# Optimization experiments

Measured on AMD Instinct MI355X. Metric: run time of the kernel, lower is better.

## Reference

```python
import jax, jax.numpy as jnp
import numpy as np

N_NODES = 50000
N_EDGES = 800000
F_IN = 128
HIDDEN = 128
N_CLASSES = 40


def setup_inputs() -> dict:
    key = jax.random.key(0)
    ks = jax.random.split(key, 8)
    x = jax.random.normal(ks[0], (N_NODES, F_IN), dtype=jnp.float32)
    edge_index = jax.random.randint(ks[1], (2, N_EDGES), 0, N_NODES, dtype=jnp.int32)
    s_in = 1.0 / np.sqrt(F_IN)
    s_h = 1.0 / np.sqrt(HIDDEN)
    W1_l = jax.random.normal(ks[2], (F_IN, HIDDEN), jnp.float32) * s_in
    W1_r = jax.random.normal(ks[3], (F_IN, HIDDEN), jnp.float32) * s_in
    b1 = jnp.zeros((HIDDEN,), jnp.float32)
    W2_l = jax.random.normal(ks[4], (HIDDEN, N_CLASSES), jnp.float32) * s_h
    W2_r = jax.random.normal(ks[5], (HIDDEN, N_CLASSES), jnp.float32) * s_h
    b2 = jnp.zeros((N_CLASSES,), jnp.float32)
    return {"x": x, "edge_index": edge_index, "W1_l": W1_l, "W1_r": W1_r,
            "b1": b1, "W2_l": W2_l, "W2_r": W2_r, "b2": b2}


def _sage_conv(x, src, dst, W_l, W_r, b):
    # mean-aggregate neighbor features at dst, then linear transform + root weight
    msg = x[src]                                                  # [E, d] gather
    agg = jax.ops.segment_sum(msg, dst, num_segments=N_NODES)     # [N, d] scatter-add
    deg = jax.ops.segment_sum(jnp.ones((src.shape[0],), x.dtype), dst,
                              num_segments=N_NODES)
    agg = agg / jnp.maximum(deg, 1.0)[:, None]                    # mean aggregation
    return agg @ W_l + x @ W_r + b


def reference(x, edge_index, W1_l, W1_r, b1, W2_l, W2_r, b2):
    src, dst = edge_index[0], edge_index[1]
    h = jax.nn.relu(_sage_conv(x, src, dst, W1_l, W1_r, b1))
    # F.dropout(p=0.5, training=self.training) -> identity in eval mode
    out = jax.nn.relu(_sage_conv(h, src, dst, W2_l, W2_r, b2))
    return jax.nn.log_softmax(out, axis=-1)
```

## Files before the change

kernel.cpp:

```cpp
#include <hip/hip_runtime.h>

#define N_NODES 50000
#define N_EDGES 800000
#define F_IN 128
#define HIDDEN 128
#define N_CLASSES 40

#define NBUCKET 196
#define BUCKET_CAP 8192
#define BINA_CHUNK 4096
#define BINA_NBLK 196
#define PREP_ITEMS (N_NODES * 32 + 128 * 256 + 80 * 128)
#define PREP_NBLK (PREP_ITEMS / 256)

#define OFF_RS     0
#define OFF_BCNT   50004
#define OFF_INVDEG 100004
#define OFF_SRCS   150004
#define OFF_AB     950004
#define OFF_PB     950004
#define OFF_Q      2950004
#define OFF_BINS   7350004
#define OFF_HB     7350004
#define OFF_WT1    10550004
#define OFF_WT2    10566388

typedef short bf16x8 __attribute__((ext_vector_type(8)));
typedef float f32x4 __attribute__((ext_vector_type(4)));
typedef unsigned short u16x8 __attribute__((ext_vector_type(8)));
typedef unsigned short u16x4 __attribute__((ext_vector_type(4)));

static __device__ __forceinline__ unsigned short f2bf(float f) {
  unsigned int u = __builtin_bit_cast(unsigned int, f);
  u = (u + 0x7fffu + ((u >> 16) & 1u)) >> 16;
  return (unsigned short)u;
}
static __device__ __forceinline__ float bf2f(unsigned short s) {
  unsigned int u = ((unsigned int)s) << 16;
  return __builtin_bit_cast(float, u);
}

__global__ __launch_bounds__(256) void k_binA_prep(
    const int* __restrict__ src, const int* __restrict__ dst,
    int* __restrict__ bcnt, int* __restrict__ bins,
    const float* __restrict__ x, const float* __restrict__ W1l,
    const float* __restrict__ W1r, const float* __restrict__ W2l,
    const float* __restrict__ W2r, unsigned short* __restrict__ Ab,
    unsigned short* __restrict__ Wt1, unsigned short* __restrict__ Wt2) {
  if (blockIdx.x >= BINA_NBLK) {
    int idx = (blockIdx.x - BINA_NBLK) * 256 + threadIdx.x;
    if (idx < N_NODES * 32) {
      int row = idx >> 5, c4 = (idx & 31) << 2;
      const float4 v = *(const float4*)(x + (size_t)row * F_IN + c4);
      ushort4 o;
      o.x = f2bf(v.x); o.y = f2bf(v.y); o.z = f2bf(v.z); o.w = f2bf(v.w);
      *(ushort4*)(Ab + (size_t)row * 256 + 128 + c4) = o;
      return;
    }
    idx -= N_NODES * 32;
    if (idx < 128 * 256) {
      int n = idx >> 8, k = idx & 255;
      float v = (k < 128) ? W1l[(size_t)k * 128 + n]
                          : W1r[(size_t)(k - 128) * 128 + n];
      Wt1[(size_t)n * 256 + k] = f2bf(v);
    } else if (idx < 128 * 256 + 80 * 128) {
      int j = idx - 128 * 256;
      int n = j >> 7, k = j & 127;
      float v = (n < 40) ? W2l[(size_t)k * 40 + n]
                         : W2r[(size_t)k * 40 + (n - 40)];
      Wt2[(size_t)n * 128 + k] = f2bf(v);
    }
    return;
  }
  __shared__ int cnt[NBUCKET];
  __shared__ int excl[NBUCKET];
  __shared__ int cursor[NBUCKET];
  __shared__ int bbase[NBUCKET];
  __shared__ int sc[256];
  __shared__ int stage[BINA_CHUNK];
  __shared__ unsigned char bkt[BINA_CHUNK];
  int t = threadIdx.x;
  int e0 = blockIdx.x * BINA_CHUNK;
  int ne = N_EDGES - e0;
  if (ne > BINA_CHUNK) ne = BINA_CHUNK;
  if (t < NBUCKET) cnt[t] = 0;
  __syncthreads();
  for (int i = t; i < ne; i += 256) atomicAdd(&cnt[dst[e0 + i] >> 8], 1);
  __syncthreads();
  int v = (t < NBUCKET) ? cnt[t] : 0;
  sc[t] = v;
  __syncthreads();
  for (int off = 1; off < 256; off <<= 1) {
    int add = (t >= off) ? sc[t - off] : 0;
    __syncthreads();
    sc[t] += add;
    __syncthreads();
  }
  if (t < NBUCKET) {
    int ex = sc[t] - v;
    excl[t] = ex;
    cursor[t] = ex;
    bbase[t] = atomicAdd(&bcnt[t], v);
  }
  __syncthreads();
  for (int i = t; i < ne; i += 256) {
    int d = dst[e0 + i];
    int s = src[e0 + i];
    int b = d >> 8;
    int pos = atomicAdd(&cursor[b], 1);
    stage[pos] = ((d & 255) << 16) | s;
    bkt[pos] = (unsigned char)b;
  }
  __syncthreads();
  for (int i = t; i < ne; i += 256) {
    int b = bkt[i];
    bins[(size_t)b * BUCKET_CAP + bbase[b] + (i - excl[b])] = stage[i];
  }
}

__global__ __launch_bounds__(256) void k_binB(
    const int* __restrict__ bcnt, const int* __restrict__ bins,
    int* __restrict__ rs, int* __restrict__ srcs,
    float* __restrict__ invdeg) {
  __shared__ int sc[256];
  __shared__ int hist[256];
  __shared__ int cursor[256];
  int b = blockIdx.x;
  int t = threadIdx.x;
  sc[t] = (t < NBUCKET && t < b) ? bcnt[t] : 0;
  __syncthreads();
  for (int off = 128; off; off >>= 1) {
    if (t < off) sc[t] += sc[t + off];
    __syncthreads();
  }
  int base = sc[0];
  int cnt = bcnt[b];
  const int* bb = bins + (size_t)b * BUCKET_CAP;
  hist[t] = 0;
  __syncthreads();
  for (int i = t; i < cnt; i += 256) atomicAdd(&hist[bb[i] >> 16], 1);
  __syncthreads();
  int c = hist[t];
  sc[t] = c;
  __syncthreads();
  for (int off = 1; off < 256; off <<= 1) {
    int add = (t >= off) ? sc[t - off] : 0;
    __syncthreads();
    sc[t] += add;
    __syncthreads();
  }
  int lexcl = sc[t] - c;
  int node = b * 256 + t;
  if (node < N_NODES) {
    rs[node] = base + lexcl;
    invdeg[node] = 1.0f / (float)(c > 1 ? c : 1);
  }
  if (b == 0 && t == 0) rs[N_NODES] = N_EDGES;
  cursor[t] = lexcl;
  __syncthreads();
  for (int i = t; i < cnt; i += 256) {
    int v = bb[i];
    int pos = atomicAdd(&cursor[v >> 16], 1);
    srcs[base + pos] = v & 0xFFFF;
  }
}

__global__ __launch_bounds__(256) void k_gather1(
    const int* __restrict__ rs, const int* __restrict__ srcs,
    const float* __restrict__ invdeg, unsigned short* __restrict__ Ab) {
  int node = blockIdx.x * 4 + (threadIdx.x >> 6);
  int lane = threadIdx.x & 63;
  int slot = lane >> 4, li = lane & 15;
  if (node >= N_NODES) return;
  int beg = rs[node], end = rs[node + 1];
  float acc[8];
#pragma unroll
  for (int j = 0; j < 8; j++) acc[j] = 0.f;
  for (int i = beg + slot; i < end; i += 4) {
    int s = srcs[i];
    u16x8 v = *(const u16x8*)(Ab + (size_t)s * 256 + 128 + li * 8);
#pragma unroll
    for (int j = 0; j < 8; j++) acc[j] += bf2f(v[j]);
  }
#pragma unroll
  for (int off = 16; off <= 32; off <<= 1)
#pragma unroll
    for (int j = 0; j < 8; j++) acc[j] += __shfl_xor(acc[j], off, 64);
  if (slot == 0) {
    float inv = invdeg[node];
    u16x8 o;
#pragma unroll
    for (int j = 0; j < 8; j++) o[j] = f2bf(acc[j] * inv);
    *(u16x8*)(Ab + (size_t)node * 256 + li * 8) = o;
  }
}

__global__ __launch_bounds__(256) void k_l1(
    const unsigned short* __restrict__ Ab, const unsigned short* __restrict__ Wt1,
    const float* __restrict__ b1, unsigned short* __restrict__ hb) {
  int w = threadIdx.x >> 6, lane = threadIdx.x & 63;
  int r = lane & 15, quad = lane >> 4;
  int row0 = blockIdx.x * 64 + w * 16;
  int arow = row0 + r;
  if (arow >= N_NODES) arow = N_NODES - 1;
  const unsigned short* Ap = Ab + (size_t)arow * 256 + quad * 8;
  const unsigned short* Bp = Wt1 + (size_t)r * 256 + quad * 8;
  f32x4 acc[8];
#pragma unroll
  for (int n = 0; n < 8; n++) acc[n] = (f32x4){0.f, 0.f, 0.f, 0.f};
#pragma unroll
  for (int k0 = 0; k0 < 256; k0 += 32) {
    bf16x8 af = *(const bf16x8*)(Ap + k0);
#pragma unroll
    for (int n = 0; n < 8; n++) {
      bf16x8 bv = *(const bf16x8*)(Bp + (size_t)n * 16 * 256 + k0);
      acc[n] = __builtin_amdgcn_mfma_f32_16x16x32_bf16(af, bv, acc[n], 0, 0, 0);
    }
  }
  int crow0 = row0 + quad * 4;
#pragma unroll
  for (int n = 0; n < 8; n++) {
    int col = n * 16 + r;
    float bias = b1[col];
#pragma unroll
    for (int reg = 0; reg < 4; reg++) {
      int row = crow0 + reg;
      if (row < N_NODES)
        hb[(size_t)row * HIDDEN + col] = f2bf(fmaxf(acc[n][reg] + bias, 0.f));
    }
  }
}

__global__ __launch_bounds__(256) void k_pq(
    const unsigned short* __restrict__ hb, const unsigned short* __restrict__ Wt2,
    const float* __restrict__ b2, unsigned short* __restrict__ pb,
    float* __restrict__ q) {
  int w = threadIdx.x >> 6, lane = threadIdx.x & 63;
  int r = lane & 15, quad = lane >> 4;
  int row0 = blockIdx.x * 64 + w * 16;
  int arow = row0 + r;
  if (arow >= N_NODES) arow = N_NODES - 1;
  const unsigned short* Ap = hb + (size_t)arow * HIDDEN + quad * 8;
  const unsigned short* Bp = Wt2 + (size_t)r * 128 + quad * 8;
  f32x4 acc[5];
#pragma unroll
  for (int n = 0; n < 5; n++) acc[n] = (f32x4){0.f, 0.f, 0.f, 0.f};
#pragma unroll
  for (int k0 = 0; k0 < 128; k0 += 32) {
    bf16x8 af = *(const bf16x8*)(Ap + k0);
#pragma unroll
    for (int n = 0; n < 5; n++) {
      bf16x8 bv = *(const bf16x8*)(Bp + (size_t)n * 16 * 128 + k0);
      acc[n] = __builtin_amdgcn_mfma_f32_16x16x32_bf16(af, bv, acc[n], 0, 0, 0);
    }
  }
  int crow0 = row0 + quad * 4;
#pragma unroll
  for (int n = 0; n < 5; n++) {
    int col = n * 16 + r;
#pragma unroll
    for (int reg = 0; reg < 4; reg++) {
      int row = crow0 + reg;
      if (row < N_NODES) {
        float v = acc[n][reg];
        if (col < N_CLASSES)
          pb[(size_t)row * 64 + col] = f2bf(v);
        else
          q[(size_t)row * N_CLASSES + (col - N_CLASSES)] = v + b2[col - N_CLASSES];
      }
    }
  }
}

__global__ __launch_bounds__(256) void k_final(
    const unsigned short* __restrict__ pb, const float* __restrict__ q,
    const int* __restrict__ rs, const int* __restrict__ srcs,
    const float* __restrict__ invdeg, float* __restrict__ out) {
  int node = blockIdx.x * 4 + (threadIdx.x >> 6);
  int lane = threadIdx.x & 63;
  int slot = lane >> 4, li = lane & 15;
  if (node >= N_NODES) return;
  int beg = rs[node], end = rs[node + 1];
  float acc[4];
#pragma unroll
  for (int j = 0; j < 4; j++) acc[j] = 0.f;
  for (int i = beg + slot; i < end; i += 4) {
    int s = srcs[i];
    u16x4 v = *(const u16x4*)(pb + (size_t)s * 64 + li * 4);
#pragma unroll
    for (int j = 0; j < 4; j++) acc[j] += bf2f(v[j]);
  }
#pragma unroll
  for (int off = 16; off <= 32; off <<= 1)
#pragma unroll
    for (int j = 0; j < 4; j++) acc[j] += __shfl_xor(acc[j], off, 64);
  float inv = invdeg[node];
  bool valid = li < 10;
  float4 qv = valid ? *(const float4*)(q + (size_t)node * N_CLASSES + li * 4)
                    : make_float4(0.f, 0.f, 0.f, 0.f);
  float v0 = valid ? fmaxf(acc[0] * inv + qv.x, 0.f) : -1e30f;
  float v1 = valid ? fmaxf(acc[1] * inv + qv.y, 0.f) : -1e30f;
  float v2 = valid ? fmaxf(acc[2] * inv + qv.z, 0.f) : -1e30f;
  float v3 = valid ? fmaxf(acc[3] * inv + qv.w, 0.f) : -1e30f;
  float m = fmaxf(fmaxf(v0, v1), fmaxf(v2, v3));
#pragma unroll
  for (int off = 1; off <= 8; off <<= 1) m = fmaxf(m, __shfl_xor(m, off, 16));
  float ssum = valid ? (__expf(v0 - m) + __expf(v1 - m) +
                        __expf(v2 - m) + __expf(v3 - m))
                     : 0.f;
#pragma unroll
  for (int off = 1; off <= 8; off <<= 1) ssum += __shfl_xor(ssum, off, 16);
  float lse = __logf(ssum) + m;
  if (slot == 0 && valid) {
    float4 o = make_float4(v0 - lse, v1 - lse, v2 - lse, v3 - lse);
    *(float4*)(out + (size_t)node * N_CLASSES + li * 4) = o;
  }
}

extern "C" void kernel_launch(void* const* d_in, const int* in_sizes, int n_in,
                              void* d_out, int out_size, void* d_ws,
                              size_t ws_size, hipStream_t stream) {
  const float* x   = (const float*)d_in[0];
  const int*   ei  = (const int*)d_in[1];
  const int*   src = ei;
  const int*   dst = ei + N_EDGES;
  const float* W1l = (const float*)d_in[2];
  const float* W1r = (const float*)d_in[3];
  const float* b1  = (const float*)d_in[4];
  const float* W2l = (const float*)d_in[5];
  const float* W2r = (const float*)d_in[6];
  const float* b2  = (const float*)d_in[7];
  float* out = (float*)d_out;

  float* wsf = (float*)d_ws;
  int*   rs     = (int*)wsf + OFF_RS;
  int*   bcnt   = (int*)wsf + OFF_BCNT;
  float* invdeg = wsf + OFF_INVDEG;
  int*   srcs   = (int*)wsf + OFF_SRCS;
  unsigned short* Ab  = (unsigned short*)(wsf + OFF_AB);
  unsigned short* pb  = (unsigned short*)(wsf + OFF_PB);
  unsigned short* hb  = (unsigned short*)(wsf + OFF_HB);
  unsigned short* Wt1 = (unsigned short*)(wsf + OFF_WT1);
  unsigned short* Wt2 = (unsigned short*)(wsf + OFF_WT2);
  int*   bins   = (int*)wsf + OFF_BINS;
  float* q = wsf + OFF_Q;

  hipMemsetAsync(bcnt, 0, NBUCKET * sizeof(int), stream);

  k_binA_prep<<<BINA_NBLK + PREP_NBLK, 256, 0, stream>>>(
      src, dst, bcnt, bins, x, W1l, W1r, W2l, W2r, Ab, Wt1, Wt2);
  k_binB<<<NBUCKET, 256, 0, stream>>>(bcnt, bins, rs, srcs, invdeg);
  k_gather1<<<(N_NODES + 3) / 4, 256, 0, stream>>>(rs, srcs, invdeg, Ab);
  k_l1<<<(N_NODES + 63) / 64, 256, 0, stream>>>(Ab, Wt1, b1, hb);
  k_pq<<<(N_NODES + 63) / 64, 256, 0, stream>>>(hb, Wt2, b2, pb, q);
  k_final<<<(N_NODES + 3) / 4, 256, 0, stream>>>(pb, q, rs, srcs, invdeg, out);
}
```

Before: 251.0 us.

## Widen gather lanes to 8 edges per wave and pack layer-2 rows densely

Both neighbor-gather kernels now give each wave eight edge slots of eight lanes instead of four slots of sixteen lanes, so more independent row loads are in flight per node. The layer-1 gather reads two 16-byte chunks per lane. The layer-2 projection buffer is packed at 40 bf16 per row (80 bytes) instead of a 64-element stride, which cuts gathered bytes, and the log-softmax reduction moves to 8-lane groups. The risks are more registers per thread, three lanes idle in each 8-lane group of the final kernel, and 80-byte rows that no longer align to cache lines.

```diff
diff --git a/kernel.cpp b/kernel.cpp
--- a/kernel.cpp
+++ b/kernel.cpp
@@ -28,7 +28,6 @@
 typedef short bf16x8 __attribute__((ext_vector_type(8)));
 typedef float f32x4 __attribute__((ext_vector_type(4)));
 typedef unsigned short u16x8 __attribute__((ext_vector_type(8)));
-typedef unsigned short u16x4 __attribute__((ext_vector_type(4)));
 
 static __device__ __forceinline__ unsigned short f2bf(float f) {
   unsigned int u = __builtin_bit_cast(unsigned int, f);
@@ -170,28 +169,37 @@
     const float* __restrict__ invdeg, unsigned short* __restrict__ Ab) {
   int node = blockIdx.x * 4 + (threadIdx.x >> 6);
   int lane = threadIdx.x & 63;
-  int slot = lane >> 4, li = lane & 15;
+  int slot = lane >> 3, li = lane & 7;
   if (node >= N_NODES) return;
   int beg = rs[node], end = rs[node + 1];
-  float acc[8];
-#pragma unroll
-  for (int j = 0; j < 8; j++) acc[j] = 0.f;
-  for (int i = beg + slot; i < end; i += 4) {
+  float acc[16];
+#pragma unroll
+  for (int j = 0; j < 16; j++) acc[j] = 0.f;
+  for (int i = beg + slot; i < end; i += 8) {
     int s = srcs[i];
-    u16x8 v = *(const u16x8*)(Ab + (size_t)s * 256 + 128 + li * 8);
-#pragma unroll
-    for (int j = 0; j < 8; j++) acc[j] += bf2f(v[j]);
-  }
-#pragma unroll
-  for (int off = 16; off <= 32; off <<= 1)
-#pragma unroll
-    for (int j = 0; j < 8; j++) acc[j] += __shfl_xor(acc[j], off, 64);
+    const unsigned short* rp = Ab + (size_t)s * 256 + 128 + li * 8;
+    u16x8 v0 = *(const u16x8*)rp;
+    u16x8 v1 = *(const u16x8*)(rp + 64);
+#pragma unroll
+    for (int j = 0; j < 8; j++) {
+      acc[j] += bf2f(v0[j]);
+      acc[8 + j] += bf2f(v1[j]);
+    }
+  }
+#pragma unroll
+  for (int off = 8; off <= 32; off <<= 1)
+#pragma unroll
+    for (int j = 0; j < 16; j++) acc[j] += __shfl_xor(acc[j], off, 64);
   if (slot == 0) {
     float inv = invdeg[node];
-    u16x8 o;
-#pragma unroll
-    for (int j = 0; j < 8; j++) o[j] = f2bf(acc[j] * inv);
-    *(u16x8*)(Ab + (size_t)node * 256 + li * 8) = o;
+    u16x8 o0, o1;
+#pragma unroll
+    for (int j = 0; j < 8; j++) {
+      o0[j] = f2bf(acc[j] * inv);
+      o1[j] = f2bf(acc[8 + j] * inv);
+    }
+    *(u16x8*)(Ab + (size_t)node * 256 + li * 8) = o0;
+    *(u16x8*)(Ab + (size_t)node * 256 + 64 + li * 8) = o1;
   }
 }
 
@@ -264,7 +272,7 @@
       if (row < N_NODES) {
         float v = acc[n][reg];
         if (col < N_CLASSES)
-          pb[(size_t)row * 64 + col] = f2bf(v);
+          pb[(size_t)row * 40 + col] = f2bf(v);
         else
           q[(size_t)row * N_CLASSES + (col - N_CLASSES)] = v + b2[col - N_CLASSES];
       }
@@ -278,42 +286,58 @@
     const float* __restrict__ invdeg, float* __restrict__ out) {
   int node = blockIdx.x * 4 + (threadIdx.x >> 6);
   int lane = threadIdx.x & 63;
-  int slot = lane >> 4, li = lane & 15;
+  int slot = lane >> 3, li = lane & 7;
   if (node >= N_NODES) return;
+  bool valid = li < 5;
   int beg = rs[node], end = rs[node + 1];
-  float acc[4];
-#pragma unroll
-  for (int j = 0; j < 4; j++) acc[j] = 0.f;
-  for (int i = beg + slot; i < end; i += 4) {
+  float acc[8];
+#pragma unroll
+  for (int j = 0; j < 8; j++) acc[j] = 0.f;
+  for (int i = beg + slot; i < end; i += 8) {
     int s = srcs[i];
-    u16x4 v = *(const u16x4*)(pb + (size_t)s * 64 + li * 4);
-#pragma unroll
-    for (int j = 0; j < 4; j++) acc[j] += bf2f(v[j]);
-  }
-#pragma unroll
-  for (int off = 16; off <= 32; off <<= 1)
-#pragma unroll
-    for (int j = 0; j < 4; j++) acc[j] += __shfl_xor(acc[j], off, 64);
+    if (valid) {
+      u16x8 v = *(const u16x8*)(pb + (size_t)s * 40 + li * 8);
+#pragma unroll
+      for (int j = 0; j < 8; j++) acc[j] += bf2f(v[j]);
+    }
+  }
+#pragma unroll
+  for (int off = 8; off <= 32; off <<= 1)
+#pragma unroll
+    for (int j = 0; j < 8; j++) acc[j] += __shfl_xor(acc[j], off, 64);
   float inv = invdeg[node];
-  bool valid = li < 10;
-  float4 qv = valid ? *(const float4*)(q + (size_t)node * N_CLASSES + li * 4)
-                    : make_float4(0.f, 0.f, 0.f, 0.f);
-  float v0 = valid ? fmaxf(acc[0] * inv + qv.x, 0.f) : -1e30f;
-  float v1 = valid ? fmaxf(acc[1] * inv + qv.y, 0.f) : -1e30f;
-  float v2 = valid ? fmaxf(acc[2] * inv + qv.z, 0.f) : -1e30f;
-  float v3 = valid ? fmaxf(acc[3] * inv + qv.w, 0.f) : -1e30f;
-  float m = fmaxf(fmaxf(v0, v1), fmaxf(v2, v3));
-#pragma unroll
-  for (int off = 1; off <= 8; off <<= 1) m = fmaxf(m, __shfl_xor(m, off, 16));
-  float ssum = valid ? (__expf(v0 - m) + __expf(v1 - m) +
-                        __expf(v2 - m) + __expf(v3 - m))
-                     : 0.f;
-#pragma unroll
-  for (int off = 1; off <= 8; off <<= 1) ssum += __shfl_xor(ssum, off, 16);
+  float v[8];
+  float m = -1e30f;
+  if (valid) {
+    const float* qr = q + (size_t)node * N_CLASSES + li * 8;
+    float4 q0 = *(const float4*)qr;
+    float4 q1 = *(const float4*)(qr + 4);
+    v[0] = fmaxf(acc[0] * inv + q0.x, 0.f);
+    v[1] = fmaxf(acc[1] * inv + q0.y, 0.f);
+    v[2] = fmaxf(acc[2] * inv + q0.z, 0.f);
+    v[3] = fmaxf(acc[3] * inv + q0.w, 0.f);
+    v[4] = fmaxf(acc[4] * inv + q1.x, 0.f);
+    v[5] = fmaxf(acc[5] * inv + q1.y, 0.f);
+    v[6] = fmaxf(acc[6] * inv + q1.z, 0.f);
+    v[7] = fmaxf(acc[7] * inv + q1.w, 0.f);
+#pragma unroll
+    for (int j = 0; j < 8; j++) m = fmaxf(m, v[j]);
+  }
+#pragma unroll
+  for (int off = 1; off <= 4; off <<= 1) m = fmaxf(m, __shfl_xor(m, off, 8));
+  float ssum = 0.f;
+  if (valid) {
+#pragma unroll
+    for (int j = 0; j < 8; j++) ssum += __expf(v[j] - m);
+  }
+#pragma unroll
+  for (int off = 1; off <= 4; off <<= 1) ssum += __shfl_xor(ssum, off, 8);
   float lse = __logf(ssum) + m;
   if (slot == 0 && valid) {
-    float4 o = make_float4(v0 - lse, v1 - lse, v2 - lse, v3 - lse);
-    *(float4*)(out + (size_t)node * N_CLASSES + li * 4) = o;
+    float* orow = out + (size_t)node * N_CLASSES + li * 8;
+    *(float4*)orow = make_float4(v[0] - lse, v[1] - lse, v[2] - lse, v[3] - lse);
+    *(float4*)(orow + 4) =
+        make_float4(v[4] - lse, v[5] - lse, v[6] - lse, v[7] - lse);
   }
 }
 
```

Result: faster. 240.6 us (-4.1%).
